# Kernel optimization log

Hardware: AMD Instinct MI355X
Metric: run time of the kernel (lower is better)

## Reference

```python
import jax, jax.numpy as jnp
import numpy as np

N_NODES = 50000
N_EDGES = 800000
D_IN = 256
D_HID = 256
N_LAYERS = 3
N_GRAPHS = 64
LN_EPS = 1e-5


def setup_inputs() -> dict:
    key = jax.random.key(0)
    ks = jax.random.split(key, 8)
    x = jax.random.normal(ks[0], (N_NODES, D_IN), dtype=jnp.float32)
    edge_index = jax.random.randint(ks[1], (2, N_EDGES), 0, N_NODES, dtype=jnp.int32)
    batch = jnp.sort(jax.random.randint(ks[2], (N_NODES,), 0, N_GRAPHS, dtype=jnp.int32))
    # GCNConv weights (glorot-ish) and biases; all layers are [D, D] since in_dim == hidden_dim
    scale = 1.0 / np.sqrt(D_IN)
    Ws = jax.random.normal(ks[3], (N_LAYERS, D_IN, D_HID), dtype=jnp.float32) * scale
    bs = jnp.zeros((N_LAYERS, D_HID), dtype=jnp.float32)
    gammas = jnp.ones((N_LAYERS, D_HID), dtype=jnp.float32)
    betas = jnp.zeros((N_LAYERS, D_HID), dtype=jnp.float32)
    return {"x": x, "edge_index": edge_index, "batch": batch,
            "Ws": Ws, "bs": bs, "gammas": gammas, "betas": betas}


def _gcn_conv(x, W, b, src, dst):
    # PyG GCNConv: h = xW; add self-loops; symmetric deg^{-1/2} normalization; scatter-add; + bias
    h = x @ W  # [N, D]
    deg = jnp.zeros((N_NODES,), dtype=x.dtype).at[dst].add(1.0) + 1.0  # +1 for self-loop
    dinv = jax.lax.rsqrt(deg)  # deg >= 1, safe
    coef = (dinv[src] * dinv[dst])[:, None]  # [E, 1]
    agg = jax.ops.segment_sum(h[src] * coef, dst, num_segments=N_NODES)
    agg = agg + h * (dinv * dinv)[:, None]  # self-loop contribution
    return agg + b


def _layer_norm(x, gamma, beta):
    mu = jnp.mean(x, axis=-1, keepdims=True)
    var = jnp.mean(jnp.square(x - mu), axis=-1, keepdims=True)
    return (x - mu) * jax.lax.rsqrt(var + LN_EPS) * gamma + beta


def reference(x, edge_index, batch, Ws, bs, gammas, betas):
    src, dst = edge_index[0], edge_index[1]
    h = x
    for l in range(N_LAYERS):
        h = _gcn_conv(h, Ws[l], bs[l], src, dst)
        h = _layer_norm(h, gammas[l], betas[l])
        h = jax.nn.relu(h)  # dropout is identity in eval mode
    # global mean pool over graphs
    sums = jax.ops.segment_sum(h, batch, num_segments=N_GRAPHS)  # [B, D]
    counts = jax.ops.segment_sum(jnp.ones((N_NODES,), dtype=h.dtype), batch, num_segments=N_GRAPHS)
    return sums / jnp.maximum(counts, 1.0)[:, None]
```

## Files before the change

kernel.cpp:

```cpp
#include <hip/hip_runtime.h>
#include <hip/hip_bf16.h>

#define N_NODES   50000
#define N_EDGES   800000
#define D         256
#define N_LAYERS  3
#define N_GRAPHS  64
#define LN_EPS    1e-5f
#define NB_SCAN   ((N_NODES + 255) / 256)
#define XT_THREADS (N_NODES * D / 8)

typedef __attribute__((ext_vector_type(8))) short bf16x8;
typedef __attribute__((ext_vector_type(4))) float f32x4;

__device__ __forceinline__ unsigned short f2bf(float f) {
    unsigned int u = __float_as_uint(f);
    unsigned int r = (u + 0x7FFFu + ((u >> 16) & 1u)) >> 16;
    return (unsigned short)r;
}
__device__ __forceinline__ float bf2f(unsigned short h) {
    return __uint_as_float(((unsigned int)h) << 16);
}

__global__ void k_convert(const float* __restrict__ x, const float* __restrict__ dinv,
                          unsigned short* __restrict__ xb,
                          const float* __restrict__ W, unsigned short* __restrict__ Wbt) {
    int gid = blockIdx.x * blockDim.x + threadIdx.x;
    if (gid < XT_THREADS) {
        int base = gid * 8;
        float sc = dinv[base >> 8];
        const float4* x4 = (const float4*)(x + base);
        float4 a = x4[0], b = x4[1];
        ushort4 lo, hi;
        lo.x = f2bf(a.x * sc); lo.y = f2bf(a.y * sc); lo.z = f2bf(a.z * sc); lo.w = f2bf(a.w * sc);
        hi.x = f2bf(b.x * sc); hi.y = f2bf(b.y * sc); hi.z = f2bf(b.z * sc); hi.w = f2bf(b.w * sc);
        ((ushort4*)(xb + base))[0] = lo;
        ((ushort4*)(xb + base))[1] = hi;
    } else {
        int g2 = gid - XT_THREADS;
        if (g2 < N_LAYERS * D * D) {
            int l = g2 >> 16;
            int rem = g2 & 65535;
            int n = rem >> 8;
            int k = rem & 255;
            Wbt[(size_t)l * D * D + n * D + k] = f2bf(W[(size_t)l * D * D + k * D + n]);
        }
    }
}

__global__ void k_indeg(const int* __restrict__ dst, int* __restrict__ indeg) {
    int e = blockIdx.x * blockDim.x + threadIdx.x;
    if (e < N_EDGES) atomicAdd(&indeg[dst[e]], 1);
}

__global__ __launch_bounds__(256) void k_dinv_bsum(const int* __restrict__ indeg,
                                                   float* __restrict__ dinv,
                                                   int* __restrict__ bsum) {
    int b = blockIdx.x, t = threadIdx.x;
    int i = b * 256 + t;
    int v = (i < N_NODES) ? indeg[i] : 0;
    if (i < N_NODES) dinv[i] = rsqrtf((float)(v + 1));
    int s = v;
#pragma unroll
    for (int m = 32; m >= 1; m >>= 1) s += __shfl_xor(s, m);
    __shared__ int sh[4];
    if ((t & 63) == 0) sh[t >> 6] = s;
    __syncthreads();
    if (t == 0) bsum[b] = sh[0] + sh[1] + sh[2] + sh[3];
}

__global__ __launch_bounds__(256) void k_bscan_counts(const int* __restrict__ bsum,
                                                      int* __restrict__ bbase,
                                                      const int* __restrict__ batch,
                                                      int* __restrict__ counts) {
    int t = threadIdx.x;
    if (t < N_GRAPHS) {
        int g = t;
        int lo = 0, hi = N_NODES;
        while (lo < hi) { int mid = (lo + hi) >> 1; if (batch[mid] < g) lo = mid + 1; else hi = mid; }
        int start = lo;
        lo = 0; hi = N_NODES;
        int g1 = g + 1;
        while (lo < hi) { int mid = (lo + hi) >> 1; if (batch[mid] < g1) lo = mid + 1; else hi = mid; }
        counts[g] = lo - start;
    }
    __shared__ int s[256];
    int v = (t < NB_SCAN) ? bsum[t] : 0;
    s[t] = v;
    __syncthreads();
    for (int off = 1; off < 256; off <<= 1) {
        int tv = (t >= off) ? s[t - off] : 0;
        __syncthreads();
        s[t] += tv;
        __syncthreads();
    }
    if (t < NB_SCAN) bbase[t] = s[t] - v;
}

__global__ __launch_bounds__(256) void k_offsets(const int* __restrict__ indeg, const int* __restrict__ bbase,
                                                 int* __restrict__ offsets, int* __restrict__ cursor) {
    __shared__ int s[256];
    int b = blockIdx.x, t = threadIdx.x;
    int i = b * 256 + t;
    int v = (i < N_NODES) ? indeg[i] : 0;
    s[t] = v;
    __syncthreads();
    for (int off = 1; off < 256; off <<= 1) {
        int tv = (t >= off) ? s[t - off] : 0;
        __syncthreads();
        s[t] += tv;
        __syncthreads();
    }
    if (i < N_NODES) {
        int o = bbase[b] + s[t] - v;
        offsets[i] = o;
        cursor[i]  = o;
    }
}

__global__ void k_csr_fill(const int* __restrict__ src, const int* __restrict__ dst,
                           int* __restrict__ cursor, unsigned short* __restrict__ esrc) {
    int e = blockIdx.x * blockDim.x + threadIdx.x;
    if (e >= N_EDGES) return;
    int s = src[e], d = dst[e];
    int pos = atomicAdd(&cursor[d], 1);
    esrc[pos] = (unsigned short)s;
}

__global__ __launch_bounds__(256) void k_layer(const unsigned short* __restrict__ hs,
                                               const int* __restrict__ offsets,
                                               const int* __restrict__ indeg,
                                               const float* __restrict__ dinv,
                                               const unsigned short* __restrict__ esrc,
                                               const unsigned short* __restrict__ Wbt,
                                               const float* __restrict__ bias,
                                               const float* __restrict__ gamma,
                                               const float* __restrict__ beta,
                                               const float* __restrict__ rowscale,
                                               unsigned short* __restrict__ out) {
    __shared__ short alds[32 * 256];
    __shared__ float red[2][4][32];
    const int t = threadIdx.x;
    const int lane = t & 63;
    const int w = t >> 6;
    const int brow = blockIdx.x * 32;

    const int hw = lane >> 5;
    const int dl = lane & 31;
    const unsigned short* hp = hs + dl * 8;

    for (int nn = 0; nn < 8; ++nn) {
        int node = brow + w * 8 + nn;
        int nodec = (node < N_NODES) ? node : (N_NODES - 1);

        float acc[8];
        if (hw == 0) {
            bf16x8 v = *(const bf16x8*)(hp + (size_t)nodec * 256);
#pragma unroll
            for (int j = 0; j < 8; ++j) acc[j] = bf2f((unsigned short)v[j]);
        } else {
#pragma unroll
            for (int j = 0; j < 8; ++j) acc[j] = 0.f;
        }

        const int beg = offsets[nodec];
        const int end = beg + indeg[nodec];
        int i = beg + hw;
        for (; i + 6 < end; i += 8) {
            int s0 = esrc[i];
            int s1 = esrc[i + 2];
            int s2 = esrc[i + 4];
            int s3 = esrc[i + 6];
            bf16x8 v0 = *(const bf16x8*)(hp + (size_t)s0 * 256);
            bf16x8 v1 = *(const bf16x8*)(hp + (size_t)s1 * 256);
            bf16x8 v2 = *(const bf16x8*)(hp + (size_t)s2 * 256);
            bf16x8 v3 = *(const bf16x8*)(hp + (size_t)s3 * 256);
#pragma unroll
            for (int j = 0; j < 8; ++j) acc[j] += bf2f((unsigned short)v0[j]);
#pragma unroll
            for (int j = 0; j < 8; ++j) acc[j] += bf2f((unsigned short)v1[j]);
#pragma unroll
            for (int j = 0; j < 8; ++j) acc[j] += bf2f((unsigned short)v2[j]);
#pragma unroll
            for (int j = 0; j < 8; ++j) acc[j] += bf2f((unsigned short)v3[j]);
        }
        for (; i < end; i += 2) {
            int s0 = esrc[i];
            bf16x8 v0 = *(const bf16x8*)(hp + (size_t)s0 * 256);
#pragma unroll
            for (int j = 0; j < 8; ++j) acc[j] += bf2f((unsigned short)v0[j]);
        }

#pragma unroll
        for (int j = 0; j < 8; ++j) acc[j] += __shfl_xor(acc[j], 32);

        if (hw == 0) {
            int r = w * 8 + nn;
            float sc = dinv[nodec];
            bf16x8 o;
#pragma unroll
            for (int j = 0; j < 8; ++j) o[j] = (short)f2bf(acc[j] * sc);
            *(bf16x8*)(alds + r * 256 + (dl ^ (r & 7)) * 8) = o;
        }
    }
    __syncthreads();

    const int lrow = lane & 15;
    const int q = lane >> 4;
    const int ncb = w * 64;

    f32x4 acc[2][4];
#pragma unroll
    for (int mt = 0; mt < 2; ++mt)
#pragma unroll
        for (int nt = 0; nt < 4; ++nt) acc[mt][nt] = (f32x4){0.f, 0.f, 0.f, 0.f};

    const unsigned short* wp = Wbt + (size_t)(ncb + lrow) * 256 + q * 8;

#pragma unroll
    for (int kh = 0; kh < 2; ++kh) {
        bf16x8 wf[4][4];
#pragma unroll
        for (int nt = 0; nt < 4; ++nt)
#pragma unroll
            for (int ks = 0; ks < 4; ++ks)
                wf[nt][ks] = *(const bf16x8*)(wp + (size_t)nt * 16 * 256 + (kh * 4 + ks) * 32);

#pragma unroll
        for (int ks = 0; ks < 4; ++ks) {
            int kk = kh * 4 + ks;
            int cs = (kk * 4 + q) ^ (lrow & 7);
#pragma unroll
            for (int mt = 0; mt < 2; ++mt) {
                bf16x8 av = *(const bf16x8*)(alds + (mt * 16 + lrow) * 256 + cs * 8);
#pragma unroll
                for (int nt = 0; nt < 4; ++nt)
                    acc[mt][nt] = __builtin_amdgcn_mfma_f32_16x16x32_bf16(wf[nt][ks], av, acc[mt][nt], 0, 0, 0);
            }
        }
    }

    const float4* bias4 = (const float4*)bias;
#pragma unroll
    for (int mt = 0; mt < 2; ++mt) {
        float s = 0.f, s2 = 0.f;
#pragma unroll
        for (int nt = 0; nt < 4; ++nt) {
            float4 bv = bias4[w * 16 + nt * 4 + q];
#pragma unroll
            for (int r = 0; r < 4; ++r) {
                float v = acc[mt][nt][r] + ((const float*)&bv)[r];
                acc[mt][nt][r] = v;
                s += v;
                s2 += v * v;
            }
        }
        s  += __shfl_xor(s, 16);  s  += __shfl_xor(s, 32);
        s2 += __shfl_xor(s2, 16); s2 += __shfl_xor(s2, 32);
        if (lane < 16) {
            red[0][w][mt * 16 + lane] = s;
            red[1][w][mt * 16 + lane] = s2;
        }
    }
    __syncthreads();

    const float4* g4 = (const float4*)gamma;
    const float4* be4 = (const float4*)beta;
#pragma unroll
    for (int mt = 0; mt < 2; ++mt) {
        int r = mt * 16 + lrow;
        float s = 0.f, s2 = 0.f;
#pragma unroll
        for (int j = 0; j < 4; ++j) { s += red[0][j][r]; s2 += red[1][j][r]; }
        float mu = s * (1.0f / 256.0f);
        float var = s2 * (1.0f / 256.0f) - mu * mu;
        float rs = rsqrtf(var + LN_EPS);

        int row = brow + r;
        if (row < N_NODES) {
            float sc = (rowscale != nullptr) ? rowscale[row] : 1.0f;
#pragma unroll
            for (int nt = 0; nt < 4; ++nt) {
                float4 gv = g4[w * 16 + nt * 4 + q];
                float4 bev = be4[w * 16 + nt * 4 + q];
                ushort4 o;
                float v0 = fmaxf((acc[mt][nt][0] - mu) * rs * gv.x + bev.x, 0.f) * sc;
                float v1 = fmaxf((acc[mt][nt][1] - mu) * rs * gv.y + bev.y, 0.f) * sc;
                float v2 = fmaxf((acc[mt][nt][2] - mu) * rs * gv.z + bev.z, 0.f) * sc;
                float v3 = fmaxf((acc[mt][nt][3] - mu) * rs * gv.w + bev.w, 0.f) * sc;
                o.x = f2bf(v0); o.y = f2bf(v1); o.z = f2bf(v2); o.w = f2bf(v3);
                *(ushort4*)(out + (size_t)row * 256 + ncb + nt * 16 + q * 4) = o;
            }
        }
    }
}

__global__ __launch_bounds__(256) void k_pool(const unsigned short* __restrict__ h,
                                              const int* __restrict__ batch,
                                              float* __restrict__ sums) {
    __shared__ int sb[128];
    int t = threadIdx.x;
    int n0 = blockIdx.x * 128;
    int cnt = N_NODES - n0; if (cnt > 128) cnt = 128;
    if (cnt <= 0) return;
    if (t < cnt) sb[t] = batch[n0 + t];
    __syncthreads();

    float acc = 0.f;
    int g = sb[0];
    for (int i = 0; i < cnt; ++i) {
        int bg = sb[i];
        if (bg != g) {
            atomicAdd(&sums[g * 256 + t], acc);
            acc = 0.f;
            g = bg;
        }
        acc += bf2f(h[(size_t)(n0 + i) * 256 + t]);
    }
    atomicAdd(&sums[g * 256 + t], acc);
}

__global__ void k_finalize(const float* __restrict__ sums, const int* __restrict__ counts,
                           float* __restrict__ out) {
    int idx = blockIdx.x * blockDim.x + threadIdx.x;
    if (idx < N_GRAPHS * 256) {
        float c = (float)counts[idx >> 8];
        out[idx] = sums[idx] / fmaxf(c, 1.f);
    }
}

extern "C" void kernel_launch(void* const* d_in, const int* in_sizes, int n_in,
                              void* d_out, int out_size, void* d_ws, size_t ws_size,
                              hipStream_t stream) {
    const float* x     = (const float*)d_in[0];
    const int*   ei    = (const int*)d_in[1];
    const int*   batch = (const int*)d_in[2];
    const float* Ws    = (const float*)d_in[3];
    const float* bs    = (const float*)d_in[4];
    const float* gammas= (const float*)d_in[5];
    const float* betas = (const float*)d_in[6];
    float* out = (float*)d_out;

    const int* src = ei;
    const int* dst = ei + N_EDGES;

    char* p = (char*)d_ws;
    unsigned short* hbfA  = (unsigned short*)p; p += (size_t)N_NODES * D * 2;
    unsigned short* hbfB  = (unsigned short*)p; p += (size_t)N_NODES * D * 2;
    unsigned short* Wbt   = (unsigned short*)p; p += (size_t)N_LAYERS * D * D * 2;
    int*   indeg  = (int*)p;   p += (size_t)N_NODES * 4;
    int*   offs   = (int*)p;   p += (size_t)N_NODES * 4;
    int*   cursor = (int*)p;   p += (size_t)N_NODES * 4;
    float* dinv   = (float*)p; p += (size_t)N_NODES * 4;
    int*   bsum   = (int*)p;   p += (size_t)NB_SCAN * 4;
    int*   bbase  = (int*)p;   p += (size_t)NB_SCAN * 4;
    unsigned short* esrc = (unsigned short*)p; p += (size_t)N_EDGES * 2;
    float* sums   = (float*)p; p += (size_t)N_GRAPHS * D * 4;
    int*   counts = (int*)p;   p += (size_t)N_GRAPHS * 4;

    hipMemsetAsync(indeg, 0, (size_t)N_NODES * 4, stream);
    hipMemsetAsync(sums, 0, (size_t)N_GRAPHS * D * 4, stream);

    k_indeg <<<(N_EDGES + 255) / 256, 256, 0, stream>>>(dst, indeg);
    k_dinv_bsum<<<NB_SCAN, 256, 0, stream>>>(indeg, dinv, bsum);
    k_convert<<<(XT_THREADS + N_LAYERS * D * D + 255) / 256, 256, 0, stream>>>(x, dinv, hbfA, Ws, Wbt);
    k_bscan_counts<<<1, 256, 0, stream>>>(bsum, bbase, batch, counts);
    k_offsets<<<NB_SCAN, 256, 0, stream>>>(indeg, bbase, offs, cursor);
    k_csr_fill<<<(N_EDGES + 255) / 256, 256, 0, stream>>>(src, dst, cursor, esrc);

    const int layer_grid = (N_NODES + 31) / 32;
    unsigned short* bufs[2] = {hbfA, hbfB};
    for (int l = 0; l < N_LAYERS; ++l) {
        const unsigned short* in_h = bufs[l & 1];
        unsigned short* out_h      = bufs[(l + 1) & 1];
        const float* rsc = (l == N_LAYERS - 1) ? nullptr : dinv;
        k_layer<<<layer_grid, 256, 0, stream>>>(in_h, offs, indeg, dinv, esrc,
                                                Wbt + (size_t)l * D * D,
                                                bs + (size_t)l * D,
                                                gammas + (size_t)l * D,
                                                betas + (size_t)l * D, rsc, out_h);
    }

    unsigned short* hfin = bufs[N_LAYERS & 1];
    k_pool<<<(N_NODES + 127) / 128, 256, 0, stream>>>(hfin, batch, sums);
    k_finalize<<<(N_GRAPHS * 256 + 255) / 256, 256, 0, stream>>>(sums, counts, out);
}
```

Measured before the change: 451.5 us.

## Split GCN layer into producer aggregation and consumer GEMM blocks synced by flags

Each layer kernel now launches nine blocks per 32-node chunk. Eight producer blocks gather neighbour features, four nodes each, and write the aggregated rows to a global buffer with cache-bypassing stores, then bump a per-chunk ready counter. A ninth consumer block spins on that counter, then runs the MFMA GEMM and the bias, LayerNorm and ReLU epilogue, reading the aggregated rows straight from global memory. The goal is more parallelism in the gather phase than the old 32-node block with 8 serial nodes per wave, and overlap of gather and GEMM across blocks. In exchange it adds an extra global round-trip of the aggregated features, relies on spin-waiting that assumes a safe block dispatch order, and drops LDS staging of the A operand.

After: 934.3 us. +106.9%, slower.

```diff
diff --git a/kernel.cpp b/kernel.cpp
--- a/kernel.cpp
+++ b/kernel.cpp
@@ -9,6 +9,7 @@
 #define LN_EPS    1e-5f
 #define NB_SCAN   ((N_NODES + 255) / 256)
 #define XT_THREADS (N_NODES * D / 8)
+#define NCHUNK    1563
 
 typedef __attribute__((ext_vector_type(8))) short bf16x8;
 typedef __attribute__((ext_vector_type(4))) float f32x4;
@@ -20,6 +21,15 @@
 }
 __device__ __forceinline__ float bf2f(unsigned short h) {
     return __uint_as_float(((unsigned int)h) << 16);
+}
+
+__device__ __forceinline__ void store_b128_sc(void* addr, bf16x8 v) {
+    asm volatile("global_store_dwordx4 %0, %1, off sc0 sc1" :: "v"(addr), "v"(v) : "memory");
+}
+__device__ __forceinline__ bf16x8 load_b128_sc(const void* addr) {
+    bf16x8 r;
+    asm volatile("global_load_dwordx4 %0, %1, off sc0 sc1" : "=v"(r) : "v"(addr) : "memory");
+    return r;
 }
 
 __global__ void k_convert(const float* __restrict__ x, const float* __restrict__ dinv,
@@ -127,169 +137,181 @@
     esrc[pos] = (unsigned short)s;
 }
 
-__global__ __launch_bounds__(256) void k_layer(const unsigned short* __restrict__ hs,
-                                               const int* __restrict__ offsets,
-                                               const int* __restrict__ indeg,
-                                               const float* __restrict__ dinv,
-                                               const unsigned short* __restrict__ esrc,
-                                               const unsigned short* __restrict__ Wbt,
-                                               const float* __restrict__ bias,
-                                               const float* __restrict__ gamma,
-                                               const float* __restrict__ beta,
-                                               const float* __restrict__ rowscale,
-                                               unsigned short* __restrict__ out) {
-    __shared__ short alds[32 * 256];
-    __shared__ float red[2][4][32];
+__global__ __launch_bounds__(256, 8) void k_layer_pc(const unsigned short* __restrict__ hs,
+                                                     const int* __restrict__ offsets,
+                                                     const int* __restrict__ indeg,
+                                                     const float* __restrict__ dinv,
+                                                     const unsigned short* __restrict__ esrc,
+                                                     unsigned short* __restrict__ aggx,
+                                                     int* __restrict__ ready,
+                                                     const unsigned short* __restrict__ Wbt,
+                                                     const float* __restrict__ bias,
+                                                     const float* __restrict__ gamma,
+                                                     const float* __restrict__ beta,
+                                                     const float* __restrict__ rowscale,
+                                                     unsigned short* __restrict__ out) {
+    const int chunk = blockIdx.x / 9;
+    const int slot  = blockIdx.x - chunk * 9;
     const int t = threadIdx.x;
     const int lane = t & 63;
-    const int w = t >> 6;
-    const int brow = blockIdx.x * 32;
-
-    const int hw = lane >> 5;
-    const int dl = lane & 31;
-    const unsigned short* hp = hs + dl * 8;
-
-    for (int nn = 0; nn < 8; ++nn) {
-        int node = brow + w * 8 + nn;
-        int nodec = (node < N_NODES) ? node : (N_NODES - 1);
-
-        float acc[8];
-        if (hw == 0) {
-            bf16x8 v = *(const bf16x8*)(hp + (size_t)nodec * 256);
-#pragma unroll
-            for (int j = 0; j < 8; ++j) acc[j] = bf2f((unsigned short)v[j]);
-        } else {
-#pragma unroll
-            for (int j = 0; j < 8; ++j) acc[j] = 0.f;
-        }
-
-        const int beg = offsets[nodec];
-        const int end = beg + indeg[nodec];
-        int i = beg + hw;
-        for (; i + 6 < end; i += 8) {
-            int s0 = esrc[i];
-            int s1 = esrc[i + 2];
-            int s2 = esrc[i + 4];
-            int s3 = esrc[i + 6];
-            bf16x8 v0 = *(const bf16x8*)(hp + (size_t)s0 * 256);
-            bf16x8 v1 = *(const bf16x8*)(hp + (size_t)s1 * 256);
-            bf16x8 v2 = *(const bf16x8*)(hp + (size_t)s2 * 256);
-            bf16x8 v3 = *(const bf16x8*)(hp + (size_t)s3 * 256);
-#pragma unroll
-            for (int j = 0; j < 8; ++j) acc[j] += bf2f((unsigned short)v0[j]);
-#pragma unroll
-            for (int j = 0; j < 8; ++j) acc[j] += bf2f((unsigned short)v1[j]);
-#pragma unroll
-            for (int j = 0; j < 8; ++j) acc[j] += bf2f((unsigned short)v2[j]);
-#pragma unroll
-            for (int j = 0; j < 8; ++j) acc[j] += bf2f((unsigned short)v3[j]);
-        }
-        for (; i < end; i += 2) {
-            int s0 = esrc[i];
-            bf16x8 v0 = *(const bf16x8*)(hp + (size_t)s0 * 256);
-#pragma unroll
-            for (int j = 0; j < 8; ++j) acc[j] += bf2f((unsigned short)v0[j]);
-        }
-
-#pragma unroll
-        for (int j = 0; j < 8; ++j) acc[j] += __shfl_xor(acc[j], 32);
-
-        if (hw == 0) {
-            int r = w * 8 + nn;
-            float sc = dinv[nodec];
-            bf16x8 o;
-#pragma unroll
-            for (int j = 0; j < 8; ++j) o[j] = (short)f2bf(acc[j] * sc);
-            *(bf16x8*)(alds + r * 256 + (dl ^ (r & 7)) * 8) = o;
-        }
-    }
-    __syncthreads();
-
-    const int lrow = lane & 15;
-    const int q = lane >> 4;
-    const int ncb = w * 64;
-
-    f32x4 acc[2][4];
-#pragma unroll
-    for (int mt = 0; mt < 2; ++mt)
-#pragma unroll
-        for (int nt = 0; nt < 4; ++nt) acc[mt][nt] = (f32x4){0.f, 0.f, 0.f, 0.f};
-
-    const unsigned short* wp = Wbt + (size_t)(ncb + lrow) * 256 + q * 8;
-
-#pragma unroll
-    for (int kh = 0; kh < 2; ++kh) {
-        bf16x8 wf[4][4];
-#pragma unroll
-        for (int nt = 0; nt < 4; ++nt)
-#pragma unroll
-            for (int ks = 0; ks < 4; ++ks)
-                wf[nt][ks] = *(const bf16x8*)(wp + (size_t)nt * 16 * 256 + (kh * 4 + ks) * 32);
-
-#pragma unroll
-        for (int ks = 0; ks < 4; ++ks) {
-            int kk = kh * 4 + ks;
-            int cs = (kk * 4 + q) ^ (lrow & 7);
-#pragma unroll
-            for (int mt = 0; mt < 2; ++mt) {
-                bf16x8 av = *(const bf16x8*)(alds + (mt * 16 + lrow) * 256 + cs * 8);
-#pragma unroll
-                for (int nt = 0; nt < 4; ++nt)
-                    acc[mt][nt] = __builtin_amdgcn_mfma_f32_16x16x32_bf16(wf[nt][ks], av, acc[mt][nt], 0, 0, 0);
-            }
-        }
-    }
-
-    const float4* bias4 = (const float4*)bias;
-#pragma unroll
-    for (int mt = 0; mt < 2; ++mt) {
-        float s = 0.f, s2 = 0.f;
-#pragma unroll
-        for (int nt = 0; nt < 4; ++nt) {
-            float4 bv = bias4[w * 16 + nt * 4 + q];
-#pragma unroll
-            for (int r = 0; r < 4; ++r) {
-                float v = acc[mt][nt][r] + ((const float*)&bv)[r];
-                acc[mt][nt][r] = v;
-                s += v;
-                s2 += v * v;
-            }
-        }
-        s  += __shfl_xor(s, 16);  s  += __shfl_xor(s, 32);
-        s2 += __shfl_xor(s2, 16); s2 += __shfl_xor(s2, 32);
-        if (lane < 16) {
-            red[0][w][mt * 16 + lane] = s;
-            red[1][w][mt * 16 + lane] = s2;
-        }
-    }
-    __syncthreads();
-
-    const float4* g4 = (const float4*)gamma;
-    const float4* be4 = (const float4*)beta;
-#pragma unroll
-    for (int mt = 0; mt < 2; ++mt) {
-        int r = mt * 16 + lrow;
-        float s = 0.f, s2 = 0.f;
-#pragma unroll
-        for (int j = 0; j < 4; ++j) { s += red[0][j][r]; s2 += red[1][j][r]; }
-        float mu = s * (1.0f / 256.0f);
-        float var = s2 * (1.0f / 256.0f) - mu * mu;
-        float rs = rsqrtf(var + LN_EPS);
-
-        int row = brow + r;
-        if (row < N_NODES) {
-            float sc = (rowscale != nullptr) ? rowscale[row] : 1.0f;
+
+    if (slot < 8) {
+        const int u = chunk * 8 + slot;
+        const int node = u * 4 + (t >> 6);
+        if (u < 12500 && node < N_NODES) {
+            const int hw = lane >> 5;
+            const int dl = lane & 31;
+            const unsigned short* hp = hs + dl * 8;
+
+            float acc[8];
+            if (hw == 0) {
+                bf16x8 v = *(const bf16x8*)(hp + (size_t)node * 256);
+#pragma unroll
+                for (int j = 0; j < 8; ++j) acc[j] = bf2f((unsigned short)v[j]);
+            } else {
+#pragma unroll
+                for (int j = 0; j < 8; ++j) acc[j] = 0.f;
+            }
+
+            const int beg = offsets[node];
+            const int end = beg + indeg[node];
+            int i = beg + hw;
+            for (; i + 6 < end; i += 8) {
+                int s0 = esrc[i];
+                int s1 = esrc[i + 2];
+                int s2 = esrc[i + 4];
+                int s3 = esrc[i + 6];
+                bf16x8 v0 = *(const bf16x8*)(hp + (size_t)s0 * 256);
+                bf16x8 v1 = *(const bf16x8*)(hp + (size_t)s1 * 256);
+                bf16x8 v2 = *(const bf16x8*)(hp + (size_t)s2 * 256);
+                bf16x8 v3 = *(const bf16x8*)(hp + (size_t)s3 * 256);
+#pragma unroll
+                for (int j = 0; j < 8; ++j) acc[j] += bf2f((unsigned short)v0[j]);
+#pragma unroll
+                for (int j = 0; j < 8; ++j) acc[j] += bf2f((unsigned short)v1[j]);
+#pragma unroll
+                for (int j = 0; j < 8; ++j) acc[j] += bf2f((unsigned short)v2[j]);
+#pragma unroll
+                for (int j = 0; j < 8; ++j) acc[j] += bf2f((unsigned short)v3[j]);
+            }
+            for (; i < end; i += 2) {
+                int s0 = esrc[i];
+                bf16x8 v0 = *(const bf16x8*)(hp + (size_t)s0 * 256);
+#pragma unroll
+                for (int j = 0; j < 8; ++j) acc[j] += bf2f((unsigned short)v0[j]);
+            }
+
+#pragma unroll
+            for (int j = 0; j < 8; ++j) acc[j] += __shfl_xor(acc[j], 32);
+
+            if (hw == 0) {
+                float sc = dinv[node];
+                bf16x8 o;
+#pragma unroll
+                for (int j = 0; j < 8; ++j) o[j] = (short)f2bf(acc[j] * sc);
+                store_b128_sc(aggx + (size_t)node * 256 + dl * 8, o);
+            }
+        }
+        asm volatile("s_waitcnt vmcnt(0)" ::: "memory");
+        __syncthreads();
+        if (t == 0) atomicAdd(&ready[chunk], 1);
+    } else {
+        __shared__ float red[2][4][32];
+        const int w = t >> 6;
+        const int lrow = lane & 15;
+        const int q = lane >> 4;
+        const int mbase = chunk * 32;
+        const int ncb = w * 64;
+
+        if (t == 0) {
+            while (atomicAdd(&ready[chunk], 0) < 8) __builtin_amdgcn_s_sleep(8);
+        }
+        __syncthreads();
+
+        int rowA[2];
+#pragma unroll
+        for (int mt = 0; mt < 2; ++mt) {
+            int r = mbase + mt * 16 + lrow;
+            rowA[mt] = (r < N_NODES) ? r : (N_NODES - 1);
+        }
+        const unsigned short* a0 = aggx + (size_t)rowA[0] * 256 + q * 8;
+        const unsigned short* a1 = aggx + (size_t)rowA[1] * 256 + q * 8;
+        const unsigned short* wp = Wbt + (size_t)(ncb + lrow) * 256 + q * 8;
+
+        f32x4 acc[2][4];
+#pragma unroll
+        for (int mt = 0; mt < 2; ++mt)
+#pragma unroll
+            for (int nt = 0; nt < 4; ++nt) acc[mt][nt] = (f32x4){0.f, 0.f, 0.f, 0.f};
+
+#pragma unroll
+        for (int kk = 0; kk < 8; ++kk) {
+            bf16x8 av0 = load_b128_sc(a0 + kk * 32);
+            bf16x8 av1 = load_b128_sc(a1 + kk * 32);
+            bf16x8 bw[4];
+#pragma unroll
+            for (int nt = 0; nt < 4; ++nt)
+                bw[nt] = *(const bf16x8*)(wp + (size_t)nt * 16 * 256 + kk * 32);
+            asm volatile("s_waitcnt vmcnt(0)" ::: "memory");
+            __builtin_amdgcn_sched_barrier(0);
 #pragma unroll
             for (int nt = 0; nt < 4; ++nt) {
-                float4 gv = g4[w * 16 + nt * 4 + q];
-                float4 bev = be4[w * 16 + nt * 4 + q];
-                ushort4 o;
-                float v0 = fmaxf((acc[mt][nt][0] - mu) * rs * gv.x + bev.x, 0.f) * sc;
-                float v1 = fmaxf((acc[mt][nt][1] - mu) * rs * gv.y + bev.y, 0.f) * sc;
-                float v2 = fmaxf((acc[mt][nt][2] - mu) * rs * gv.z + bev.z, 0.f) * sc;
-                float v3 = fmaxf((acc[mt][nt][3] - mu) * rs * gv.w + bev.w, 0.f) * sc;
-                o.x = f2bf(v0); o.y = f2bf(v1); o.z = f2bf(v2); o.w = f2bf(v3);
-                *(ushort4*)(out + (size_t)row * 256 + ncb + nt * 16 + q * 4) = o;
+                acc[0][nt] = __builtin_amdgcn_mfma_f32_16x16x32_bf16(bw[nt], av0, acc[0][nt], 0, 0, 0);
+                acc[1][nt] = __builtin_amdgcn_mfma_f32_16x16x32_bf16(bw[nt], av1, acc[1][nt], 0, 0, 0);
+            }
+        }
+
+        const float4* bias4 = (const float4*)bias;
+#pragma unroll
+        for (int mt = 0; mt < 2; ++mt) {
+            float s = 0.f, s2 = 0.f;
+#pragma unroll
+            for (int nt = 0; nt < 4; ++nt) {
+                float4 bv = bias4[w * 16 + nt * 4 + q];
+#pragma unroll
+                for (int r = 0; r < 4; ++r) {
+                    float v = acc[mt][nt][r] + ((const float*)&bv)[r];
+                    acc[mt][nt][r] = v;
+                    s += v;
+                    s2 += v * v;
+                }
+            }
+            s  += __shfl_xor(s, 16);  s  += __shfl_xor(s, 32);
+            s2 += __shfl_xor(s2, 16); s2 += __shfl_xor(s2, 32);
+            if (lane < 16) {
+                red[0][w][mt * 16 + lane] = s;
+                red[1][w][mt * 16 + lane] = s2;
+            }
+        }
+        __syncthreads();
+
+        const float4* g4 = (const float4*)gamma;
+        const float4* be4 = (const float4*)beta;
+#pragma unroll
+        for (int mt = 0; mt < 2; ++mt) {
+            int r = mt * 16 + lrow;
+            float s = 0.f, s2 = 0.f;
+#pragma unroll
+            for (int j = 0; j < 4; ++j) { s += red[0][j][r]; s2 += red[1][j][r]; }
+            float mu = s * (1.0f / 256.0f);
+            float var = s2 * (1.0f / 256.0f) - mu * mu;
+            float rs = rsqrtf(var + LN_EPS);
+
+            int row = mbase + r;
+            if (row < N_NODES) {
+                float sc = (rowscale != nullptr) ? rowscale[row] : 1.0f;
+#pragma unroll
+                for (int nt = 0; nt < 4; ++nt) {
+                    float4 gv = g4[w * 16 + nt * 4 + q];
+                    float4 bev = be4[w * 16 + nt * 4 + q];
+                    ushort4 o;
+                    float v0 = fmaxf((acc[mt][nt][0] - mu) * rs * gv.x + bev.x, 0.f) * sc;
+                    float v1 = fmaxf((acc[mt][nt][1] - mu) * rs * gv.y + bev.y, 0.f) * sc;
+                    float v2 = fmaxf((acc[mt][nt][2] - mu) * rs * gv.z + bev.z, 0.f) * sc;
+                    float v3 = fmaxf((acc[mt][nt][3] - mu) * rs * gv.w + bev.w, 0.f) * sc;
+                    o.x = f2bf(v0); o.y = f2bf(v1); o.z = f2bf(v2); o.w = f2bf(v3);
+                    *(ushort4*)(out + (size_t)row * 256 + ncb + nt * 16 + q * 4) = o;
+                }
             }
         }
     }
@@ -347,6 +369,7 @@
     char* p = (char*)d_ws;
     unsigned short* hbfA  = (unsigned short*)p; p += (size_t)N_NODES * D * 2;
     unsigned short* hbfB  = (unsigned short*)p; p += (size_t)N_NODES * D * 2;
+    unsigned short* aggx  = (unsigned short*)p; p += (size_t)N_NODES * D * 2;
     unsigned short* Wbt   = (unsigned short*)p; p += (size_t)N_LAYERS * D * D * 2;
     int*   indeg  = (int*)p;   p += (size_t)N_NODES * 4;
     int*   offs   = (int*)p;   p += (size_t)N_NODES * 4;
@@ -357,9 +380,11 @@
     unsigned short* esrc = (unsigned short*)p; p += (size_t)N_EDGES * 2;
     float* sums   = (float*)p; p += (size_t)N_GRAPHS * D * 4;
     int*   counts = (int*)p;   p += (size_t)N_GRAPHS * 4;
+    int*   ready3 = (int*)p;   p += (size_t)3 * NCHUNK * 4;
 
     hipMemsetAsync(indeg, 0, (size_t)N_NODES * 4, stream);
     hipMemsetAsync(sums, 0, (size_t)N_GRAPHS * D * 4, stream);
+    hipMemsetAsync(ready3, 0, (size_t)3 * NCHUNK * 4, stream);
 
     k_indeg <<<(N_EDGES + 255) / 256, 256, 0, stream>>>(dst, indeg);
     k_dinv_bsum<<<NB_SCAN, 256, 0, stream>>>(indeg, dinv, bsum);
@@ -368,13 +393,14 @@
     k_offsets<<<NB_SCAN, 256, 0, stream>>>(indeg, bbase, offs, cursor);
     k_csr_fill<<<(N_EDGES + 255) / 256, 256, 0, stream>>>(src, dst, cursor, esrc);
 
-    const int layer_grid = (N_NODES + 31) / 32;
+    const int pc_grid = NCHUNK * 9;
     unsigned short* bufs[2] = {hbfA, hbfB};
     for (int l = 0; l < N_LAYERS; ++l) {
         const unsigned short* in_h = bufs[l & 1];
         unsigned short* out_h      = bufs[(l + 1) & 1];
         const float* rsc = (l == N_LAYERS - 1) ? nullptr : dinv;
-        k_layer<<<layer_grid, 256, 0, stream>>>(in_h, offs, indeg, dinv, esrc,
+        k_layer_pc<<<pc_grid, 256, 0, stream>>>(in_h, offs, indeg, dinv, esrc,
+                                                aggx, ready3 + l * NCHUNK,
                                                 Wbt + (size_t)l * D * D,
                                                 bs + (size_t)l * D,
                                                 gammas + (size_t)l * D,
```
